# Optimization experiments

Measured on AMD Instinct MI355X. Metric: run time of the kernel, lower is better.

Reference implementation:

```python
import jax, jax.numpy as jnp
import numpy as np

SCALE = 2

def setup_inputs() -> dict:
    key = jax.random.key(0)
    ks = jax.random.split(key, 8)
    b, c, h, w = 4, 64, 128, 128
    C = c * SCALE * SCALE  # 256
    Cq = C // 8            # 32
    return {
        "x": jax.random.normal(ks[0], (b, c, h, w), dtype=jnp.float32),
        "wq": jax.random.normal(ks[1], (Cq, C), dtype=jnp.float32) * 0.05,
        "bq": jax.random.normal(ks[2], (Cq,), dtype=jnp.float32) * 0.05,
        "wk": jax.random.normal(ks[3], (Cq, C), dtype=jnp.float32) * 0.05,
        "bk": jax.random.normal(ks[4], (Cq,), dtype=jnp.float32) * 0.05,
        "wv": jax.random.normal(ks[5], (C, C), dtype=jnp.float32) * 0.05,
        "bv": jax.random.normal(ks[6], (C,), dtype=jnp.float32) * 0.05,
        "gamma": jax.random.normal(ks[7], (1,), dtype=jnp.float32) * 0.1,
    }

def _space_to_depth(x, s):
    # faithful to the torch permute/view chain: (b,c,h,w) -> (b, c*s*s, h//s, w//s)
    b, c, h, w = x.shape
    xp = jnp.transpose(x, (0, 3, 2, 1)).reshape(b, w, h // s, c * s)
    xp = jnp.transpose(xp, (0, 2, 1, 3)).reshape(b, h // s, w // s, c * s * s)
    return jnp.transpose(xp, (0, 3, 1, 2))

def _depth_to_space(y, s):
    # inverse rearrange: (b, C, H, W) -> (b, C//(s*s), H*s, W*s)
    B, C, H, W = y.shape
    yp = jnp.transpose(y, (0, 2, 3, 1)).reshape(B, H, W * s, C // s)
    yp = jnp.transpose(yp, (0, 2, 1, 3)).reshape(B, W * s, H * s, C // (s * s))
    return jnp.transpose(yp, (0, 3, 2, 1))

def reference(x, wq, bq, wk, bk, wv, bv, gamma):
    s = SCALE
    xp = _space_to_depth(x, s)            # (B, C, H, W)
    B, C, H, W = xp.shape
    N = H * W
    # 1x1 convs as channel matmuls
    q = jnp.einsum('bchw,oc->bohw', xp, wq) + bq[None, :, None, None]
    k = jnp.einsum('bchw,oc->bohw', xp, wk) + bk[None, :, None, None]
    v = jnp.einsum('bchw,oc->bohw', xp, wv) + bv[None, :, None, None]
    q = q.reshape(B, -1, N)               # (B, Cq, N)
    k = k.reshape(B, -1, N)               # (B, Cq, N)
    v = v.reshape(B, C, N)                # (B, C, N)
    energy = jnp.einsum('bcn,bcm->bnm', q, k)          # (B, N, N), no scaling (faithful)
    attention = jax.nn.softmax(energy, axis=-1)
    out = jnp.einsum('bcm,bnm->bcn', v, attention)     # value @ attention^T
    out = out.reshape(B, C, H, W)
    out = gamma * out + xp
    return _depth_to_space(out, s)        # back to (b, c, h, w)
```

## Files before the change

### kernel.cpp

```cpp
#include <hip/hip_runtime.h>

typedef __bf16 bf16_t;
typedef __bf16 bf16x2 __attribute__((ext_vector_type(2)));
typedef __bf16 bf16x8 __attribute__((ext_vector_type(8)));
typedef float  f32x4  __attribute__((ext_vector_type(4)));
typedef float  f32x16 __attribute__((ext_vector_type(16)));
typedef unsigned u32x4 __attribute__((ext_vector_type(4)));

#define HIN 128
#define WIN 128
#define LOG2E 1.4426950408889634f

__device__ __forceinline__ unsigned pk(float a, float b) {
    bf16x2 v; v[0] = (bf16_t)a; v[1] = (bf16_t)b;
    return __builtin_bit_cast(unsigned, v);
}

__device__ __forceinline__ void glds16(const bf16_t* g, bf16_t* l) {
    __builtin_amdgcn_global_load_lds(
        (const __attribute__((address_space(1))) unsigned int*)g,
        (__attribute__((address_space(3))) unsigned int*)l, 16, 0, 0);
}

__device__ __forceinline__ bf16x8 cvt8(const float* p) {
    float4 w0 = *(const float4*)p;
    float4 w1 = *(const float4*)(p + 4);
    bf16x8 r = { (bf16_t)w0.x, (bf16_t)w0.y, (bf16_t)w0.z, (bf16_t)w0.w,
                 (bf16_t)w1.x, (bf16_t)w1.y, (bf16_t)w1.z, (bf16_t)w1.w };
    return r;
}

__global__ __launch_bounds__(256) void proj_kernel(
    const float* __restrict__ x,
    const float* __restrict__ wq, const float* __restrict__ bq,
    const float* __restrict__ wk, const float* __restrict__ bk,
    const float* __restrict__ wv, const float* __restrict__ bv,
    bf16_t* __restrict__ Qg, bf16_t* __restrict__ Kg, bf16_t* __restrict__ Vg)
{
    __shared__ __attribute__((aligned(16))) bf16_t Xs[32 * 256];
    const int blk  = blockIdx.x;
    const int half = blk & 1;
    const int h2   = (blk >> 1) & 63;
    const int b    = blk >> 7;
    const int tid  = threadIdx.x;

    const float* xb = x + ((size_t)b << 20);
    for (int s = 0; s < 8; ++s) {
        int v   = tid + (s << 8);
        int cin = v >> 5;
        int hb  = (v >> 4) & 1;
        int w4l = v & 15;
        const float4 xv = *(const float4*)(xb + ((size_t)cin * HIN + (2*h2 + hb)) * WIN
                                           + ((half * 16 + w4l) << 2));
        float vals[4] = {xv.x, xv.y, xv.z, xv.w};
        #pragma unroll
        for (int j = 0; j < 4; ++j) {
            int nl = ((w4l << 2) + j) >> 1;
            int c  = ((j & 1) << 7) + (hb << 6) + cin;
            int chunk = c >> 3;
            int phys  = chunk ^ (nl & 7);
            Xs[(nl << 8) + (phys << 3) + (c & 7)] = (bf16_t)vals[j];
        }
    }
    __syncthreads();

    const int ln = tid & 63;
    const int w  = tid >> 6;
    const int l  = ln & 15;
    const int q  = ln >> 4;
    const int nbase = h2 * 64 + half * 32;

    for (int it = 0; it < 5; ++it) {
        int ot = w * 5 + it;
        if (ot < 4) {
            const float* W  = (ot < 2) ? wq : wk;
            const float* Bp = (ot < 2) ? bq : bk;
            int o0 = (ot & 1) * 16;
            float4 b4 = *(const float4*)&Bp[o0 + q * 4];
            f32x4 acc[2];
            #pragma unroll
            for (int nt = 0; nt < 2; ++nt) {
                acc[nt][0] = b4.x; acc[nt][1] = b4.y;
                acc[nt][2] = b4.z; acc[nt][3] = b4.w;
            }
            for (int ks = 0; ks < 8; ++ks) {
                bf16x8 aw = cvt8(W + (size_t)(o0 + l) * 256 + (ks << 5) + (q << 3));
                #pragma unroll
                for (int nt = 0; nt < 2; ++nt) {
                    int phys = ((ks << 2) + q) ^ (l & 7);
                    const bf16x8 bx = *(const bf16x8*)&Xs[((nt * 16 + l) << 8) + (phys << 3)];
                    acc[nt] = __builtin_amdgcn_mfma_f32_16x16x32_bf16(aw, bx, acc[nt], 0, 0, 0);
                }
            }
            bf16_t* dst = (ot < 2) ? Qg : Kg;
            #pragma unroll
            for (int nt = 0; nt < 2; ++nt) {
                int n = nbase + nt * 16 + l;
                uint2 dv;
                dv.x = pk(acc[nt][0], acc[nt][1]);
                dv.y = pk(acc[nt][2], acc[nt][3]);
                *(uint2*)(dst + (((size_t)(b * 4096 + n)) << 5) + o0 + q * 4) = dv;
            }
        } else {
            int c0 = (ot - 4) * 16;
            float bias = bv[c0 + l];
            f32x4 acc[2];
            #pragma unroll
            for (int nt = 0; nt < 2; ++nt) {
                acc[nt][0] = bias; acc[nt][1] = bias;
                acc[nt][2] = bias; acc[nt][3] = bias;
            }
            for (int ks = 0; ks < 8; ++ks) {
                bf16x8 bw = cvt8(wv + (size_t)(c0 + l) * 256 + (ks << 5) + (q << 3));
                #pragma unroll
                for (int nt = 0; nt < 2; ++nt) {
                    int phys = ((ks << 2) + q) ^ (l & 7);
                    const bf16x8 ax = *(const bf16x8*)&Xs[((nt * 16 + l) << 8) + (phys << 3)];
                    acc[nt] = __builtin_amdgcn_mfma_f32_16x16x32_bf16(ax, bw, acc[nt], 0, 0, 0);
                }
            }
            int mloc = 4 * (q >> 1) + 8 * (q & 1);
            #pragma unroll
            for (int nt = 0; nt < 2; ++nt) {
                int nhi = (nbase + nt * 16 + (mloc & 8)) >> 3;
                uint2 dv;
                dv.x = pk(acc[nt][0], acc[nt][1]);
                dv.y = pk(acc[nt][2], acc[nt][3]);
                *(uint2*)(Vg + ((size_t)(b * 512 + nhi) << 11)
                             + ((c0 + l) << 3) + (mloc & 4)) = dv;
            }
        }
    }
}

__global__ __launch_bounds__(256, 2) void attn_kernel(
    const bf16_t* __restrict__ Qg, const bf16_t* __restrict__ Kg,
    const bf16_t* __restrict__ Vg, bf16_t* __restrict__ Pp,
    float* __restrict__ Lp, int T, int S)
{
    __shared__ __attribute__((aligned(16))) bf16_t Vs[2][16384];
    __shared__ __attribute__((aligned(16))) bf16_t Ksh[2][2048];

    const int blk = blockIdx.x;
    int b, qt, s;
    if (S == 4) {
        int xcd = blk & 7;
        b = xcd >> 1;
        int g = blk >> 3;
        qt = g >> 1;
        s  = (xcd & 1) * 2 + (g & 1);
    } else {
        b = blk & 3;
        int rest = blk >> 2;
        qt = rest & 31;
        s  = rest >> 5;
    }
    const int n0 = qt * 128;

    const int tid  = threadIdx.x;
    const int wv   = tid >> 6;
    const int p    = wv & 1;
    const int ch   = wv >> 1;
    const int lane = tid & 63;
    const int i    = lane & 31;
    const int h    = lane >> 5;

    const bf16_t* Qb = Qg + ((size_t)b << 17);
    const bf16_t* Kb = Kg + ((size_t)b << 17);
    const bf16_t* Vb = Vg + ((size_t)b << 20);

    bf16x8 Qf[2][2];
    #pragma unroll
    for (int qg = 0; qg < 2; ++qg)
        #pragma unroll
        for (int dc = 0; dc < 2; ++dc)
            Qf[qg][dc] = *(const bf16x8*)(Qb + (size_t)(n0 + p * 64 + qg * 32 + i) * 32
                                             + dc * 16 + h * 8);

    f32x16 acc[2][4];
    #pragma unroll
    for (int qg = 0; qg < 2; ++qg)
        #pragma unroll
        for (int cb = 0; cb < 4; ++cb)
            #pragma unroll
            for (int r = 0; r < 16; ++r) acc[qg][cb][r] = 0.f;
    float lrow[2] = {0.f, 0.f};
    const f32x16 z16 = acc[0][0];

    auto stage = [&](int buf, int m0) {
        const bf16_t* vsrc = Vb + ((size_t)(m0 >> 3) << 11);
        #pragma unroll
        for (int r = 0; r < 8; ++r) {
            int wcb = r * 4 + wv;
            glds16(vsrc + ((size_t)(wcb >> 2) << 11) + ((wcb & 3) << 9) + lane * 8,
                   &Vs[buf][(wcb << 9)] );
        }
        glds16(Kb + (size_t)(m0 + lane) * 32 + wv * 8, &Ksh[buf][wv << 9]);
    };

    stage(0, s * T * 64);

    for (int t = 0; t < T; ++t) {
        __asm__ volatile("s_waitcnt vmcnt(0)" ::: "memory");
        __asm__ volatile("s_barrier" ::: "memory");

        if (t + 1 < T)
            stage((t + 1) & 1, (s * T + t + 1) * 64);

        const bf16_t* Vt = Vs[t & 1];
        const bf16_t* Kt = Ksh[t & 1];

        bf16x8 Pf[2][4];
        #pragma unroll
        for (int qg = 0; qg < 2; ++qg) {
            f32x16 sT[2];
            #pragma unroll
            for (int mb = 0; mb < 2; ++mb) {
                int m = mb * 32 + i;
                bf16x8 kf0 = *(const bf16x8*)&Kt[((h * 64) + m) * 8];
                bf16x8 kf1 = *(const bf16x8*)&Kt[(((2 + h) * 64) + m) * 8];
                sT[mb] = __builtin_amdgcn_mfma_f32_32x32x16_bf16(kf0, Qf[qg][0], z16, 0, 0, 0);
                sT[mb] = __builtin_amdgcn_mfma_f32_32x32x16_bf16(kf1, Qf[qg][1], sT[mb], 0, 0, 0);
            }
            float psum = 0.f;
            #pragma unroll
            for (int mb = 0; mb < 2; ++mb)
                #pragma unroll
                for (int r = 0; r < 16; ++r) {
                    float pv = __builtin_amdgcn_exp2f(
                        __builtin_fmaf(sT[mb][r], LOG2E, -28.0f));
                    sT[mb][r] = pv;
                    psum += pv;
                }
            lrow[qg] += psum;
            #pragma unroll
            for (int mc = 0; mc < 4; ++mc) {
                int mb = mc >> 1, base = (mc & 1) * 8;
                u32x4 u;
                u[0] = pk(sT[mb][base + 0], sT[mb][base + 1]);
                u[1] = pk(sT[mb][base + 2], sT[mb][base + 3]);
                u[2] = pk(sT[mb][base + 4], sT[mb][base + 5]);
                u[3] = pk(sT[mb][base + 6], sT[mb][base + 7]);
                Pf[qg][mc] = __builtin_bit_cast(bf16x8, u);
            }
        }

        #pragma unroll
        for (int mc = 0; mc < 4; ++mc) {
            int mc8 = 2 * mc + h;
            #pragma unroll
            for (int cb = 0; cb < 4; ++cb) {
                int c = ch * 128 + cb * 32 + i;
                const bf16x8 Vf = *(const bf16x8*)&Vt[(mc8 << 11) + (c << 3)];
                #pragma unroll
                for (int qg = 0; qg < 2; ++qg)
                    acc[qg][cb] = __builtin_amdgcn_mfma_f32_32x32x16_bf16(Vf, Pf[qg][mc], acc[qg][cb], 0, 0, 0);
            }
        }
    }

    #pragma unroll
    for (int qg = 0; qg < 2; ++qg)
        lrow[qg] += __shfl_xor(lrow[qg], 32);

    const size_t pb = ((size_t)(s * 4 + b)) << 20;
    #pragma unroll
    for (int qg = 0; qg < 2; ++qg) {
        const int n = n0 + p * 64 + qg * 32 + i;
        bf16_t* prow = Pp + pb + ((size_t)n << 8);
        #pragma unroll
        for (int cb = 0; cb < 4; ++cb) {
            #pragma unroll
            for (int g = 0; g < 4; ++g) {
                int c_base = ch * 128 + cb * 32 + g * 8 + h * 4;
                uint2 dv;
                dv.x = pk(acc[qg][cb][g * 4 + 0], acc[qg][cb][g * 4 + 1]);
                dv.y = pk(acc[qg][cb][g * 4 + 2], acc[qg][cb][g * 4 + 3]);
                *(uint2*)(prow + c_base) = dv;
            }
        }
        if (h == 0 && ch == 0)
            Lp[((size_t)(s * 4 + b) << 12) + n] = lrow[qg];
    }
}

__global__ __launch_bounds__(256) void epi_kernel(
    const bf16_t* __restrict__ Pp, const float* __restrict__ Lp,
    const float* __restrict__ x, const float* __restrict__ gamma,
    float* __restrict__ out, int S)
{
    __shared__ __attribute__((aligned(16))) float Os[32 * 256];
    __shared__ float winv[32];
    const int blk  = blockIdx.x;
    const int half = blk & 1;
    const int h2   = (blk >> 1) & 63;
    const int b    = blk >> 7;
    const int tid  = threadIdx.x;
    const int nbase = h2 * 64 + half * 32;

    if (tid < 32) {
        int n = nbase + tid;
        float L = 0.f;
        for (int s = 0; s < S; ++s)
            L += Lp[((size_t)(s * 4 + b) << 12) + n];
        winv[tid] = 1.0f / L;
    }
    __syncthreads();

    for (int it = 0; it < 4; ++it) {
        int v  = tid + (it << 8);
        int i  = v >> 5;
        int ch = v & 31;
        int n  = nbase + i;
        float fo[8] = {0.f,0.f,0.f,0.f,0.f,0.f,0.f,0.f};
        for (int s = 0; s < S; ++s) {
            bf16x8 pv = *(const bf16x8*)(Pp + ((size_t)(s * 4 + b) << 20)
                                            + ((size_t)n << 8) + (ch << 3));
            #pragma unroll
            for (int e8 = 0; e8 < 8; ++e8) fo[e8] += (float)pv[e8];
        }
        float wn = winv[i];
        #pragma unroll
        for (int e8 = 0; e8 < 8; ++e8) fo[e8] *= wn;
        #pragma unroll
        for (int hh = 0; hh < 2; ++hh) {
            int f = (ch << 1) + hh;
            int phys = f ^ (i & 15) ^ ((f >> 3) & 4);
            *(float4*)&Os[(i << 8) + (phys << 2)] =
                float4{fo[hh*4+0], fo[hh*4+1], fo[hh*4+2], fo[hh*4+3]};
        }
    }
    __syncthreads();

    const float g = gamma[0];
    const float* xb = x + ((size_t)b << 20);
    float* ob       = out + ((size_t)b << 20);
    for (int it = 0; it < 8; ++it) {
        int uu  = tid + (it << 8);
        int e4  = uu >> 7;
        int h1b = (uu >> 6) & 1;
        int w1l = uu & 63;
        int i   = w1l >> 1;
        int f   = ((w1l & 1) << 5) | (h1b << 4) | e4;
        int phys = f ^ (i & 15) ^ ((f >> 3) & 4);
        float4 ov = *(const float4*)&Os[(i << 8) + (phys << 2)];
        float vals[4] = {ov.x, ov.y, ov.z, ov.w};
        int w1 = (half << 6) + w1l;
        #pragma unroll
        for (int k = 0; k < 4; ++k) {
            int e  = (e4 << 2) + k;
            int xi = (e * HIN + (2 * h2 + h1b)) * WIN + w1;
            ob[xi] = g * vals[k] + xb[xi];
        }
    }
}

extern "C" void kernel_launch(void* const* d_in, const int* in_sizes, int n_in,
                              void* d_out, int out_size, void* d_ws, size_t ws_size,
                              hipStream_t stream) {
    const float* x  = (const float*)d_in[0];
    const float* wq = (const float*)d_in[1];
    const float* bq = (const float*)d_in[2];
    const float* wk = (const float*)d_in[3];
    const float* bk = (const float*)d_in[4];
    const float* wv = (const float*)d_in[5];
    const float* bv = (const float*)d_in[6];
    const float* gm = (const float*)d_in[7];
    float* out = (float*)d_out;

    char* ws = (char*)d_ws;
    bf16_t* Qg = (bf16_t*)(ws);
    bf16_t* Kg = (bf16_t*)(ws + (1u << 20));
    bf16_t* Vg = (bf16_t*)(ws + (2u << 20));
    const size_t pp_off = (size_t)10 << 20;

    int S = 1;
    if (pp_off + 2 * (((size_t)8 << 20) + ((size_t)128 << 10)) <= ws_size) S = 2;
    if (pp_off + 4 * (((size_t)8 << 20) + ((size_t)128 << 10)) <= ws_size) S = 4;
    bf16_t* Pp = (bf16_t*)(ws + pp_off);
    float*  Lp = (float*)(ws + pp_off + (size_t)S * ((size_t)8 << 20));
    int T = 64 / S;

    hipLaunchKernelGGL(proj_kernel, dim3(512), dim3(256), 0, stream,
                       x, wq, bq, wk, bk, wv, bv, Qg, Kg, Vg);
    hipLaunchKernelGGL(attn_kernel, dim3(128 * S), dim3(256), 0, stream,
                       Qg, Kg, Vg, Pp, Lp, T, S);
    hipLaunchKernelGGL(epi_kernel, dim3(512), dim3(256), 0, stream,
                       Pp, Lp, x, gm, out, S);
}
```

Measured before the change: 173.3 us.

## Give each wave 32 query rows across all 256 channels instead of 64x128 split

Changes the per-wave work split in the attention kernel so each of the 4 waves owns a distinct 32-row query group and all 256 value channels, rather than pairs of waves sharing 64 queries and splitting channels. This removes the duplicated QK^T MFMAs and exp2 work that two waves previously computed for the same query rows, halving score/softmax computation per block. In exchange each V fragment read from LDS now feeds only one MFMA instead of two, doubling LDS traffic for V per MFMA.

After: 156.5 us. -9.7%, faster.

```diff
diff --git a/kernel.cpp b/kernel.cpp
--- a/kernel.cpp
+++ b/kernel.cpp
@@ -159,8 +159,6 @@
 
     const int tid  = threadIdx.x;
     const int wv   = tid >> 6;
-    const int p    = wv & 1;
-    const int ch   = wv >> 1;
     const int lane = tid & 63;
     const int i    = lane & 31;
     const int h    = lane >> 5;
@@ -169,23 +167,18 @@
     const bf16_t* Kb = Kg + ((size_t)b << 17);
     const bf16_t* Vb = Vg + ((size_t)b << 20);
 
-    bf16x8 Qf[2][2];
+    bf16x8 Qf[2];
     #pragma unroll
-    for (int qg = 0; qg < 2; ++qg)
-        #pragma unroll
-        for (int dc = 0; dc < 2; ++dc)
-            Qf[qg][dc] = *(const bf16x8*)(Qb + (size_t)(n0 + p * 64 + qg * 32 + i) * 32
-                                             + dc * 16 + h * 8);
-
-    f32x16 acc[2][4];
+    for (int dc = 0; dc < 2; ++dc)
+        Qf[dc] = *(const bf16x8*)(Qb + (size_t)(n0 + wv * 32 + i) * 32 + dc * 16 + h * 8);
+
+    f32x16 acc[8];
     #pragma unroll
-    for (int qg = 0; qg < 2; ++qg)
-        #pragma unroll
-        for (int cb = 0; cb < 4; ++cb)
-            #pragma unroll
-            for (int r = 0; r < 16; ++r) acc[qg][cb][r] = 0.f;
-    float lrow[2] = {0.f, 0.f};
-    const f32x16 z16 = acc[0][0];
+    for (int cb = 0; cb < 8; ++cb)
+        #pragma unroll
+        for (int r = 0; r < 16; ++r) acc[cb][r] = 0.f;
+    float lrow = 0.f;
+    const f32x16 z16 = acc[0];
 
     auto stage = [&](int buf, int m0) {
         const bf16_t* vsrc = Vb + ((size_t)(m0 >> 3) << 11);
@@ -193,7 +186,7 @@
         for (int r = 0; r < 8; ++r) {
             int wcb = r * 4 + wv;
             glds16(vsrc + ((size_t)(wcb >> 2) << 11) + ((wcb & 3) << 9) + lane * 8,
-                   &Vs[buf][(wcb << 9)] );
+                   &Vs[buf][(wcb << 9)]);
         }
         glds16(Kb + (size_t)(m0 + lane) * 32 + wv * 8, &Ksh[buf][wv << 9]);
     };
@@ -210,78 +203,70 @@
         const bf16_t* Vt = Vs[t & 1];
         const bf16_t* Kt = Ksh[t & 1];
 
-        bf16x8 Pf[2][4];
-        #pragma unroll
-        for (int qg = 0; qg < 2; ++qg) {
-            f32x16 sT[2];
-            #pragma unroll
-            for (int mb = 0; mb < 2; ++mb) {
-                int m = mb * 32 + i;
-                bf16x8 kf0 = *(const bf16x8*)&Kt[((h * 64) + m) * 8];
-                bf16x8 kf1 = *(const bf16x8*)&Kt[(((2 + h) * 64) + m) * 8];
-                sT[mb] = __builtin_amdgcn_mfma_f32_32x32x16_bf16(kf0, Qf[qg][0], z16, 0, 0, 0);
-                sT[mb] = __builtin_amdgcn_mfma_f32_32x32x16_bf16(kf1, Qf[qg][1], sT[mb], 0, 0, 0);
-            }
-            float psum = 0.f;
-            #pragma unroll
-            for (int mb = 0; mb < 2; ++mb)
-                #pragma unroll
-                for (int r = 0; r < 16; ++r) {
-                    float pv = __builtin_amdgcn_exp2f(
-                        __builtin_fmaf(sT[mb][r], LOG2E, -28.0f));
-                    sT[mb][r] = pv;
-                    psum += pv;
-                }
-            lrow[qg] += psum;
-            #pragma unroll
-            for (int mc = 0; mc < 4; ++mc) {
-                int mb = mc >> 1, base = (mc & 1) * 8;
-                u32x4 u;
-                u[0] = pk(sT[mb][base + 0], sT[mb][base + 1]);
-                u[1] = pk(sT[mb][base + 2], sT[mb][base + 3]);
-                u[2] = pk(sT[mb][base + 4], sT[mb][base + 5]);
-                u[3] = pk(sT[mb][base + 6], sT[mb][base + 7]);
-                Pf[qg][mc] = __builtin_bit_cast(bf16x8, u);
-            }
+        f32x16 sT[2];
+        #pragma unroll
+        for (int mb = 0; mb < 2; ++mb) {
+            int m = mb * 32 + i;
+            bf16x8 kf0 = *(const bf16x8*)&Kt[((h * 64) + m) * 8];
+            bf16x8 kf1 = *(const bf16x8*)&Kt[(((2 + h) * 64) + m) * 8];
+            sT[mb] = __builtin_amdgcn_mfma_f32_32x32x16_bf16(kf0, Qf[0], z16, 0, 0, 0);
+            sT[mb] = __builtin_amdgcn_mfma_f32_32x32x16_bf16(kf1, Qf[1], sT[mb], 0, 0, 0);
+        }
+
+        float psum = 0.f;
+        #pragma unroll
+        for (int mb = 0; mb < 2; ++mb)
+            #pragma unroll
+            for (int r = 0; r < 16; ++r) {
+                float pv = __builtin_amdgcn_exp2f(
+                    __builtin_fmaf(sT[mb][r], LOG2E, -28.0f));
+                sT[mb][r] = pv;
+                psum += pv;
+            }
+        lrow += psum;
+
+        bf16x8 Pf[4];
+        #pragma unroll
+        for (int mc = 0; mc < 4; ++mc) {
+            int mb = mc >> 1, base = (mc & 1) * 8;
+            u32x4 u;
+            u[0] = pk(sT[mb][base + 0], sT[mb][base + 1]);
+            u[1] = pk(sT[mb][base + 2], sT[mb][base + 3]);
+            u[2] = pk(sT[mb][base + 4], sT[mb][base + 5]);
+            u[3] = pk(sT[mb][base + 6], sT[mb][base + 7]);
+            Pf[mc] = __builtin_bit_cast(bf16x8, u);
         }
 
         #pragma unroll
         for (int mc = 0; mc < 4; ++mc) {
             int mc8 = 2 * mc + h;
             #pragma unroll
-            for (int cb = 0; cb < 4; ++cb) {
-                int c = ch * 128 + cb * 32 + i;
+            for (int cb = 0; cb < 8; ++cb) {
+                int c = cb * 32 + i;
                 const bf16x8 Vf = *(const bf16x8*)&Vt[(mc8 << 11) + (c << 3)];
-                #pragma unroll
-                for (int qg = 0; qg < 2; ++qg)
-                    acc[qg][cb] = __builtin_amdgcn_mfma_f32_32x32x16_bf16(Vf, Pf[qg][mc], acc[qg][cb], 0, 0, 0);
-            }
-        }
-    }
-
+                acc[cb] = __builtin_amdgcn_mfma_f32_32x32x16_bf16(Vf, Pf[mc], acc[cb], 0, 0, 0);
+            }
+        }
+    }
+
+    lrow += __shfl_xor(lrow, 32);
+
+    const size_t pb = ((size_t)(s * 4 + b)) << 20;
+    const int n = n0 + wv * 32 + i;
+    bf16_t* prow = Pp + pb + ((size_t)n << 8);
     #pragma unroll
-    for (int qg = 0; qg < 2; ++qg)
-        lrow[qg] += __shfl_xor(lrow[qg], 32);
-
-    const size_t pb = ((size_t)(s * 4 + b)) << 20;
-    #pragma unroll
-    for (int qg = 0; qg < 2; ++qg) {
-        const int n = n0 + p * 64 + qg * 32 + i;
-        bf16_t* prow = Pp + pb + ((size_t)n << 8);
-        #pragma unroll
-        for (int cb = 0; cb < 4; ++cb) {
-            #pragma unroll
-            for (int g = 0; g < 4; ++g) {
-                int c_base = ch * 128 + cb * 32 + g * 8 + h * 4;
-                uint2 dv;
-                dv.x = pk(acc[qg][cb][g * 4 + 0], acc[qg][cb][g * 4 + 1]);
-                dv.y = pk(acc[qg][cb][g * 4 + 2], acc[qg][cb][g * 4 + 3]);
-                *(uint2*)(prow + c_base) = dv;
-            }
-        }
-        if (h == 0 && ch == 0)
-            Lp[((size_t)(s * 4 + b) << 12) + n] = lrow[qg];
-    }
+    for (int cb = 0; cb < 8; ++cb) {
+        #pragma unroll
+        for (int g = 0; g < 4; ++g) {
+            int c_base = cb * 32 + g * 8 + h * 4;
+            uint2 dv;
+            dv.x = pk(acc[cb][g * 4 + 0], acc[cb][g * 4 + 1]);
+            dv.y = pk(acc[cb][g * 4 + 2], acc[cb][g * 4 + 3]);
+            *(uint2*)(prow + c_base) = dv;
+        }
+    }
+    if (h == 0)
+        Lp[((size_t)(s * 4 + b) << 12) + n] = lrow;
 }
 
 __global__ __launch_bounds__(256) void epi_kernel(
```
